# Kernel optimization log

Measured on AMD Instinct MI355X. Metric: run time of the kernel, lower is better.

The kernel has to match this reference:

```python
import jax, jax.numpy as jnp
from jax import lax
import numpy as np

G = 33            # LUT grid size per axis (hard-coded in module)
G3 = G * G * G    # 35937 entries per channel LUT


def _gelu(x):
    return jax.nn.gelu(x, approximate=False)  # torch nn.GELU default = exact erf


def _conv(x, w, b):
    # 3x3 stride-1 padding-1 conv == SAME padding, NCHW/OIHW like torch
    y = lax.conv_general_dilated(x, w, (1, 1), 'SAME',
                                 dimension_numbers=('NCHW', 'OIHW', 'NCHW'))
    return y + b[None, :, None, None]


def _bn(x, g, b, eps=1e-5):
    # eval-mode BatchNorm2d with running_mean=0, running_var=1
    s = g * (1.0 + eps) ** -0.5
    return x * s[None, :, None, None] + b[None, :, None, None]


def _resblock(x, wA, bA, gA, btA, wB, bB, gB, btB):
    h = _gelu(_bn(_conv(x, wA, bA), gA, btA))
    h = _bn(_conv(h, wB, bB), gB, btB)
    return _gelu(h + x)


def _apply_luts(luts_flat, recon):
    # Trilinear 3D-LUT sampling == F.grid_sample(mode='bilinear', padding_mode='border',
    # align_corners=True) on a 5D LUT. grid = recon[...,[2,1,0]]*2-1 means image ch0 (R)
    # indexes LUT dim 2, ch1 (G) dim 3, ch2 (B) dim 4; align_corners maps v->v*(G-1).
    # luts_flat: [B, L*3, G^3] (all num_luts fused into the channel dim, gathered once)
    # recon:     [B, 3, H, W] in [0,1]
    B, C3, _ = luts_flat.shape
    _, _, H, W = recon.shape
    c = jnp.clip(recon * (G - 1.0), 0.0, G - 1.0)      # border clamp
    f0 = jnp.clip(jnp.floor(c), 0.0, G - 2.0)
    t = c - f0                                          # fractional weights [B,3,H,W]
    i0 = f0.astype(jnp.int32)
    r0, g0, b0 = i0[:, 0], i0[:, 1], i0[:, 2]           # [B,H,W] each
    tr, tg, tb = t[:, 0], t[:, 1], t[:, 2]
    out = jnp.zeros((B, C3, H * W), dtype=luts_flat.dtype)
    for dr in (0, 1):
        for dg in (0, 1):
            for db in (0, 1):
                idx = ((r0 + dr) * G + (g0 + dg)) * G + (b0 + db)   # [B,H,W]
                w = ((tr if dr else 1.0 - tr) * (tg if dg else 1.0 - tg)
                     * (tb if db else 1.0 - tb))
                vals = jnp.take_along_axis(luts_flat, idx.reshape(B, 1, H * W), axis=2)
                out = out + vals * w.reshape(B, 1, H * W)
    return out.reshape(B, C3 // 3, 3, H, W)            # [B, L, 3, H, W]


def setup_inputs() -> dict:
    key = jax.random.key(0)
    ks = iter(jax.random.split(key, 32))
    def nrm(shape, s=0.02):
        return jax.random.normal(next(ks), shape, jnp.float32) * s
    B, T, V, E, HID, L, H, W = 4, 1024, 1024, 256, 256, 8, 384, 384
    inp = dict(
        tokens=jax.random.randint(next(ks), (B, T), 0, V),
        img=jax.random.uniform(next(ks), (B, 3, H, W), jnp.float32),
        recon_image=jax.random.uniform(next(ks), (B, 3, H, W), jnp.float32),
        emb_table=nrm((V, E)),
        agg_w1=nrm((E, HID)), agg_b1=jnp.zeros((HID,), jnp.float32),
        agg_w2=nrm((HID, HID)), agg_b2=jnp.zeros((HID,), jnp.float32),
        lut_w1=nrm((HID, HID)), lut_b1=jnp.zeros((HID,), jnp.float32),
        lut_w2=nrm((HID, L * 3 * G3), 0.005),
        lut_b2=jnp.zeros((L * 3 * G3,), jnp.float32),
        wg_w1=nrm((HID, HID // 4)), wg_b1=jnp.zeros((HID // 4,), jnp.float32),
        wg_w2=nrm((HID // 4, L)), wg_b2=jnp.zeros((L,), jnp.float32),
        rp_cin_w=nrm((32, 3, 3, 3)), rp_cin_b=jnp.zeros((32,), jnp.float32),
        rp_rbA_w=nrm((32, 32, 3, 3)), rp_rbA_b=jnp.zeros((32,), jnp.float32),
        rp_rbA_g=jnp.ones((32,), jnp.float32), rp_rbA_bt=jnp.zeros((32,), jnp.float32),
        rp_rbB_w=nrm((32, 32, 3, 3)), rp_rbB_b=jnp.zeros((32,), jnp.float32),
        rp_rbB_g=jnp.ones((32,), jnp.float32), rp_rbB_bt=jnp.zeros((32,), jnp.float32),
        rp_cout_w=nrm((3, 32, 3, 3)), rp_cout_b=jnp.zeros((3,), jnp.float32),
        fu_cin_w=nrm((32, 6, 3, 3)), fu_cin_b=jnp.zeros((32,), jnp.float32),
        fu_rbA_w=nrm((32, 32, 3, 3)), fu_rbA_b=jnp.zeros((32,), jnp.float32),
        fu_rbA_g=jnp.ones((32,), jnp.float32), fu_rbA_bt=jnp.zeros((32,), jnp.float32),
        fu_rbB_w=nrm((32, 32, 3, 3)), fu_rbB_b=jnp.zeros((32,), jnp.float32),
        fu_rbB_g=jnp.ones((32,), jnp.float32), fu_rbB_bt=jnp.zeros((32,), jnp.float32),
        fu_cout_w=nrm((3, 32, 3, 3)), fu_cout_b=jnp.zeros((3,), jnp.float32),
    )
    return inp


def reference(tokens, img, recon_image, emb_table,
              agg_w1, agg_b1, agg_w2, agg_b2,
              lut_w1, lut_b1, lut_w2, lut_b2,
              wg_w1, wg_b1, wg_w2, wg_b2,
              rp_cin_w, rp_cin_b, rp_rbA_w, rp_rbA_b, rp_rbA_g, rp_rbA_bt,
              rp_rbB_w, rp_rbB_b, rp_rbB_g, rp_rbB_bt, rp_cout_w, rp_cout_b,
              fu_cin_w, fu_cin_b, fu_rbA_w, fu_rbA_b, fu_rbA_g, fu_rbA_bt,
              fu_rbB_w, fu_rbB_b, fu_rbB_g, fu_rbB_bt, fu_cout_w, fu_cout_b):
    B = img.shape[0]
    L = wg_w2.shape[1]
    # token features
    emb = emb_table[tokens]                       # [B, T, E]
    tf = jnp.mean(emb, axis=1)                    # [B, E]
    tf = _gelu(tf @ agg_w1 + agg_b1) @ agg_w2 + agg_b2   # [B, HID]
    # dynamic LUTs and fusion weights
    lut_params = _gelu(tf @ lut_w1 + lut_b1) @ lut_w2 + lut_b2   # [B, L*3*G3]
    luts_flat = lut_params.reshape(B, L * 3, G3)
    lw = jax.nn.softmax(_gelu(tf @ wg_w1 + wg_b1) @ wg_w2 + wg_b2, axis=1)  # [B, L]
    # apply all LUTs in one fused gather pass, then weighted sum over LUTs
    lut_out = _apply_luts(luts_flat, recon_image)                # [B, L, 3, H, W]
    fused = jnp.einsum('blchw,bl->bchw', lut_out, lw)            # [B, 3, H, W]
    # residual processing branch on original img
    proc = _gelu(_conv(img, rp_cin_w, rp_cin_b))
    proc = _resblock(proc, rp_rbA_w, rp_rbA_b, rp_rbA_g, rp_rbA_bt,
                     rp_rbB_w, rp_rbB_b, rp_rbB_g, rp_rbB_bt)
    proc = _conv(proc, rp_cout_w, rp_cout_b)
    # fusion
    comb = jnp.concatenate([fused, proc], axis=1)                # [B, 6, H, W]
    out = _gelu(_conv(comb, fu_cin_w, fu_cin_b))
    out = _resblock(out, fu_rbA_w, fu_rbA_b, fu_rbA_g, fu_rbA_bt,
                    fu_rbB_w, fu_rbB_b, fu_rbB_g, fu_rbB_bt)
    out = _conv(out, fu_cout_w, fu_cout_b)
    return out + img
```

## Files before the change

### kernel.cpp

```cpp
#include <hip/hip_runtime.h>
#include <hip/hip_bf16.h>
#include <math.h>

#define BB    4
#define TT    1024
#define EE    256
#define HIDD  256
#define LLUT  8
#define HGT   384
#define WID   384
#define HWPX  147456
#define GSZ   33
#define G3    35937
#define NCOL  862488

typedef __attribute__((ext_vector_type(8))) short bf16x8;
typedef __attribute__((ext_vector_type(4))) float f32x4;

__device__ __forceinline__ float gelu_f(float x) {
    float s = 1.5957691216057308f * x * (1.0f + 0.044715f * x * x);
    float e = __expf(s);
    return x - x / (e + 1.0f);
}

__device__ __forceinline__ ushort f2bf(float x) {
    uint u = __float_as_uint(x);
    return (ushort)((u + 0x7FFFu + ((u >> 16) & 1u)) >> 16);
}
__device__ __forceinline__ uint pack2bf(float a, float b) {
    return (uint)f2bf(a) | ((uint)f2bf(b) << 16);
}
__device__ __forceinline__ float bf2f_lo(uint u) { return __uint_as_float(u << 16); }
__device__ __forceinline__ float bf2f_hi(uint u) { return __uint_as_float(u & 0xFFFF0000u); }

__global__ __launch_bounds__(256) void emb_partial_kernel(
    const int* __restrict__ tokens, const float* __restrict__ emb,
    float* __restrict__ partial)
{
    const int s = blockIdx.x, b = blockIdx.y, tid = threadIdx.x;
    const int* tok = tokens + b * TT + s * 16;
    float acc = 0.f;
#pragma unroll
    for (int t = 0; t < 16; ++t) acc += emb[tok[t] * EE + tid];
    partial[(b * 64 + s) * EE + tid] = acc;
}

__global__ __launch_bounds__(1024) void mlp_head_kernel(
    const float* __restrict__ partial,
    const float* __restrict__ aw1, const float* __restrict__ ab1,
    const float* __restrict__ aw2, const float* __restrict__ ab2,
    const float* __restrict__ lw1, const float* __restrict__ lb1,
    const float* __restrict__ gw1, const float* __restrict__ gb1,
    const float* __restrict__ gw2, const float* __restrict__ gb2,
    float* __restrict__ h3_out, float* __restrict__ lw_out)
{
    const int b = blockIdx.x;
    const int tid = threadIdx.x;
    const int o = tid & 255;
    const int q = tid >> 8;
    __shared__ float tf[256], h1[256], tf2s[256], h4[64], lg[8];
    __shared__ float red[4][256];

    {
        float acc = 0.f;
#pragma unroll
        for (int s = 0; s < 16; ++s)
            acc += partial[(b * 64 + q * 16 + s) * EE + o];
        red[q][o] = acc;
    }
    __syncthreads();
    if (tid < 256)
        tf[tid] = (red[0][tid] + red[1][tid] + red[2][tid] + red[3][tid]) * (1.0f / TT);
    __syncthreads();

    {
        float s = 0.f;
#pragma unroll 8
        for (int j = 0; j < 64; ++j) {
            const int k = (q << 6) + j;
            s += tf[k] * aw1[k * HIDD + o];
        }
        red[q][o] = s;
    }
    __syncthreads();
    if (tid < 256)
        h1[tid] = gelu_f(red[0][tid] + red[1][tid] + red[2][tid] + red[3][tid] + ab1[tid]);
    __syncthreads();

    {
        float s = 0.f;
#pragma unroll 8
        for (int j = 0; j < 64; ++j) {
            const int k = (q << 6) + j;
            s += h1[k] * aw2[k * HIDD + o];
        }
        red[q][o] = s;
    }
    __syncthreads();
    if (tid < 256)
        tf2s[tid] = red[0][tid] + red[1][tid] + red[2][tid] + red[3][tid] + ab2[tid];
    __syncthreads();

    {
        float s = 0.f;
#pragma unroll 8
        for (int j = 0; j < 64; ++j) {
            const int k = (q << 6) + j;
            s += tf2s[k] * lw1[k * HIDD + o];
        }
        red[q][o] = s;
    }
    __syncthreads();
    if (tid < 256)
        h3_out[b * HIDD + tid] =
            gelu_f(red[0][tid] + red[1][tid] + red[2][tid] + red[3][tid] + lb1[tid]);
    __syncthreads();

    {
        const int o64 = tid & 63, q16 = tid >> 6;
        float s = 0.f;
#pragma unroll
        for (int j = 0; j < 16; ++j) {
            const int k = q16 * 16 + j;
            s += tf2s[k] * gw1[k * 64 + o64];
        }
        ((float*)red)[q16 * 64 + o64] = s;
    }
    __syncthreads();
    if (tid < 64) {
        float s = gb1[tid];
#pragma unroll
        for (int r = 0; r < 16; ++r) s += ((float*)red)[r * 64 + tid];
        h4[tid] = gelu_f(s);
    }
    __syncthreads();

    if (tid < 8) {
        float s = gb2[tid];
#pragma unroll 8
        for (int k = 0; k < 64; ++k) s += h4[k] * gw2[k * LLUT + tid];
        lg[tid] = s;
    }
    __syncthreads();
    if (tid == 0) {
        float m = lg[0];
        for (int i = 1; i < LLUT; ++i) m = fmaxf(m, lg[i]);
        float ssum = 0.f, ex[LLUT];
        for (int i = 0; i < LLUT; ++i) { ex[i] = expf(lg[i] - m); ssum += ex[i]; }
        for (int i = 0; i < LLUT; ++i) lw_out[b * LLUT + i] = ex[i] / ssum;
    }
}

__global__ __launch_bounds__(256) void lut_gemm_kernel(
    const float* __restrict__ h3, const float* __restrict__ w2,
    const float* __restrict__ b2, float* __restrict__ lp)
{
    __shared__ float h[BB * HIDD];
    const int tid = threadIdx.x;
    for (int i = tid; i < BB * HIDD; i += 256) h[i] = h3[i];
    __syncthreads();

    const long col = ((long)blockIdx.x * 256 + tid) * 4;
    if (col >= NCOL) return;

    const float4 bias = *(const float4*)(b2 + col);
    float4 a0 = bias, a1 = bias, a2 = bias, a3 = bias;
    const float* wp = w2 + col;
#pragma unroll 4
    for (int k = 0; k < HIDD; ++k) {
        float4 w = *(const float4*)(wp + (long)k * NCOL);
        float h0 = h[k], h1v = h[HIDD + k], h2 = h[2 * HIDD + k], h3v = h[3 * HIDD + k];
        a0.x += h0 * w.x;  a0.y += h0 * w.y;  a0.z += h0 * w.z;  a0.w += h0 * w.w;
        a1.x += h1v * w.x; a1.y += h1v * w.y; a1.z += h1v * w.z; a1.w += h1v * w.w;
        a2.x += h2 * w.x;  a2.y += h2 * w.y;  a2.z += h2 * w.z;  a2.w += h2 * w.w;
        a3.x += h3v * w.x; a3.y += h3v * w.y; a3.z += h3v * w.z; a3.w += h3v * w.w;
    }
    *(float4*)(lp + 0L * NCOL + col) = a0;
    *(float4*)(lp + 1L * NCOL + col) = a1;
    *(float4*)(lp + 2L * NCOL + col) = a2;
    *(float4*)(lp + 3L * NCOL + col) = a3;
}

__global__ __launch_bounds__(256) void combine_kernel(
    const float* __restrict__ lp, const float* __restrict__ lwv,
    float* __restrict__ clut)
{
    const int v = blockIdx.x * 256 + threadIdx.x;
    const int b = blockIdx.y;
    if (v >= G3) return;
    float w[LLUT];
#pragma unroll
    for (int l = 0; l < LLUT; ++l) w[l] = lwv[b * LLUT + l];
#pragma unroll
    for (int c = 0; c < 3; ++c) {
        float s = 0.f;
#pragma unroll
        for (int l = 0; l < LLUT; ++l)
            s += w[l] * lp[(long)b * NCOL + (long)(l * 3 + c) * G3 + v];
        clut[(long)(b * 3 + c) * G3 + v] = s;
    }
}

__global__ __launch_bounds__(256) void applylut_out3_kernel(
    const float* __restrict__ clut, const float* __restrict__ recon,
    const ushort* __restrict__ act2, const float* __restrict__ wgt,
    const float* __restrict__ bias, float* __restrict__ comb)
{
    const int p = blockIdx.x * 256 + threadIdx.x;
    const int b = blockIdx.y;

    const float* rc = recon + (long)b * 3 * HWPX;
    float cr = fminf(fmaxf(rc[p] * 32.f, 0.f), 32.f);
    float cg = fminf(fmaxf(rc[HWPX + p] * 32.f, 0.f), 32.f);
    float cb = fminf(fmaxf(rc[2 * HWPX + p] * 32.f, 0.f), 32.f);
    float fr = fminf(floorf(cr), 31.f);
    float fg = fminf(floorf(cg), 31.f);
    float fb = fminf(floorf(cb), 31.f);
    float tr = cr - fr, tg = cg - fg, tb_ = cb - fb;
    int idx = (((int)fr * GSZ + (int)fg) * GSZ + (int)fb);
    float c[3];
#pragma unroll
    for (int ch = 0; ch < 3; ++ch) {
        const float* lut = clut + (long)(b * 3 + ch) * G3;
        float v000 = lut[idx],                  v001 = lut[idx + 1];
        float v010 = lut[idx + GSZ],            v011 = lut[idx + GSZ + 1];
        float v100 = lut[idx + GSZ * GSZ],      v101 = lut[idx + GSZ * GSZ + 1];
        float v110 = lut[idx + GSZ * GSZ + GSZ], v111 = lut[idx + GSZ * GSZ + GSZ + 1];
        float c00 = v000 + (v001 - v000) * tb_;
        float c01 = v010 + (v011 - v010) * tb_;
        float c10 = v100 + (v101 - v100) * tb_;
        float c11 = v110 + (v111 - v110) * tb_;
        float c0 = c00 + (c01 - c00) * tg;
        float c1 = c10 + (c11 - c10) * tg;
        c[ch] = c0 + (c1 - c0) * tr;
    }
    float4 r4; r4.x = c[0]; r4.y = c[1]; r4.z = c[2]; r4.w = 0.f;
    *(float4*)(comb + ((long)b * HWPX + p) * 8) = r4;

    const int hh = p / WID, ww = p - hh * WID;
    float acc[3] = {bias[0], bias[1], bias[2]};
#pragma unroll
    for (int tap = 0; tap < 9; ++tap) {
        const int dh = tap / 3, dw = tap - dh * 3;
        const int gh = hh + dh - 1, gw = ww + dw - 1;
        if (gh < 0 || gh >= HGT || gw < 0 || gw >= WID) continue;
        const uint4* xp = (const uint4*)(act2 + ((long)b * HWPX + gh * WID + gw) * 32);
        float xx[32];
#pragma unroll
        for (int q = 0; q < 4; ++q) {
            uint4 v = xp[q];
            xx[q * 8 + 0] = bf2f_lo(v.x); xx[q * 8 + 1] = bf2f_hi(v.x);
            xx[q * 8 + 2] = bf2f_lo(v.y); xx[q * 8 + 3] = bf2f_hi(v.y);
            xx[q * 8 + 4] = bf2f_lo(v.z); xx[q * 8 + 5] = bf2f_hi(v.z);
            xx[q * 8 + 6] = bf2f_lo(v.w); xx[q * 8 + 7] = bf2f_hi(v.w);
        }
#pragma unroll
        for (int o = 0; o < 3; ++o)
#pragma unroll
            for (int ci = 0; ci < 32; ++ci)
                acc[o] += xx[ci] * wgt[o * 288 + ci * 9 + tap];
    }
    float4 s4; s4.x = acc[0]; s4.y = acc[1]; s4.z = acc[2]; s4.w = 0.f;
    *(float4*)(comb + ((long)b * HWPX + p) * 8 + 4) = s4;
}

__global__ __launch_bounds__(256) void conv_in3_kernel(
    const float* __restrict__ img, const float* __restrict__ wgt,
    const float* __restrict__ bias, ushort* __restrict__ out)
{
    const int tid = threadIdx.x;
    const int p0 = (blockIdx.x * 256 + tid) * 2;
    const int b = blockIdx.y;
    const int hh = p0 / WID, ww = p0 - hh * WID;

    float acc[32][2];
#pragma unroll
    for (int o = 0; o < 32; ++o) { float bv = bias[o]; acc[o][0] = bv; acc[o][1] = bv; }

    const bool wlo = (ww > 0), whi = (ww + 2 < WID);
#pragma unroll
    for (int ci = 0; ci < 3; ++ci) {
        const float* ip = img + (long)(b * 3 + ci) * HWPX;
        float x[3][4];
#pragma unroll
        for (int dh = 0; dh < 3; ++dh) {
            const int hs = hh + dh - 1;
            const bool hok = (hs >= 0) && (hs < HGT);
            const float* rp_ = ip + hs * WID + ww;
            x[dh][0] = (hok && wlo) ? rp_[-1] : 0.f;
            x[dh][1] = hok ? rp_[0] : 0.f;
            x[dh][2] = hok ? rp_[1] : 0.f;
            x[dh][3] = (hok && whi) ? rp_[2] : 0.f;
        }
#pragma unroll
        for (int o = 0; o < 32; ++o) {
            const float* wv = wgt + o * 27 + ci * 9;
#pragma unroll
            for (int dh = 0; dh < 3; ++dh)
#pragma unroll
                for (int dw = 0; dw < 3; ++dw) {
                    const float w = wv[dh * 3 + dw];
                    acc[o][0] += x[dh][dw]     * w;
                    acc[o][1] += x[dh][dw + 1] * w;
                }
        }
    }

    ushort* op = out + ((long)b * HWPX + p0) * 32;
#pragma unroll
    for (int px = 0; px < 2; ++px) {
        uint u[16];
#pragma unroll
        for (int o2 = 0; o2 < 16; ++o2)
            u[o2] = pack2bf(gelu_f(acc[2 * o2][px]), gelu_f(acc[2 * o2 + 1][px]));
        uint4* dst = (uint4*)(op + px * 32);
#pragma unroll
        for (int q = 0; q < 4; ++q)
            dst[q] = make_uint4(u[4 * q], u[4 * q + 1], u[4 * q + 2], u[4 * q + 3]);
    }
}

#define TH2 8
#define TW2 64
#define HALO_H2 10
#define HALO_W2 66
#define CSTR 40

template <bool HAS_RES>
__global__ __launch_bounds__(512, 4) void conv32_mfma(
    const ushort* __restrict__ in, const ushort* __restrict__ res,
    const float* __restrict__ wgt, const float* __restrict__ bias,
    const float* __restrict__ bn_g, const float* __restrict__ bn_bt,
    ushort* __restrict__ out)
{
    __shared__ ushort halo[HALO_H2 * HALO_W2 * CSTR];
    __shared__ ushort wlA[9 * 2 * 64 * 8];
    __shared__ float s_scale[32], s_shift[32];

    const int tid = threadIdx.x;
    const int b  = blockIdx.z;
    const int h0 = blockIdx.y * TH2;
    const int w0 = blockIdx.x * TW2;

    for (int i = tid; i < 9 * 2 * 64 * 8; i += 512) {
        const int j    = i & 7;
        const int lane_= (i >> 3) & 63;
        const int half = (i >> 9) & 1;
        const int tap  = i >> 10;
        const int co = half * 16 + (lane_ & 15);
        const int ci = (lane_ >> 4) * 8 + j;
        wlA[i] = f2bf(wgt[co * 288 + ci * 9 + tap]);
    }
    if (tid < 32) {
        float sg = bn_g[tid] * 0.9999950000375f;
        s_scale[tid] = sg;
        s_shift[tid] = bias[tid] * sg + bn_bt[tid];
    }

    const ushort* inb = in + (long)b * HWPX * 32;
    for (int i = tid; i < HALO_H2 * HALO_W2 * 4; i += 512) {
        const int row = i / (HALO_W2 * 4);
        const int rem = i - row * (HALO_W2 * 4);
        const int px = rem >> 2, q = rem & 3;
        const int gh = h0 + row - 1, gw = w0 + px - 1;
        uint4 v = make_uint4(0u, 0u, 0u, 0u);
        if (gh >= 0 && gh < HGT && gw >= 0 && gw < WID)
            v = *(const uint4*)(inb + ((long)gh * WID + gw) * 32 + q * 8);
        *(uint4*)(&halo[(row * HALO_W2 + px) * CSTR + q * 8]) = v;
    }
    __syncthreads();

    const int lane = tid & 63, wid = tid >> 6;
    const int l15 = lane & 15, kg = lane >> 4;
    const int r = wid;

    f32x4 acc[4][2];
#pragma unroll
    for (int f = 0; f < 4; ++f)
#pragma unroll
        for (int cf = 0; cf < 2; ++cf)
            acc[f][cf] = (f32x4){0.f, 0.f, 0.f, 0.f};

#pragma unroll
    for (int tap = 0; tap < 9; ++tap) {
        const int dh = tap / 3, dw = tap - dh * 3;
        const bf16x8 a0 = *(const bf16x8*)(&wlA[((tap * 2 + 0) * 64 + lane) * 8]);
        const bf16x8 a1 = *(const bf16x8*)(&wlA[((tap * 2 + 1) * 64 + lane) * 8]);
#pragma unroll
        for (int f = 0; f < 4; ++f) {
            const int c0 = f * 16;
            const bf16x8 bfv = *(const bf16x8*)(
                &halo[((r + dh) * HALO_W2 + (c0 + dw + l15)) * CSTR + kg * 8]);
            acc[f][0] = __builtin_amdgcn_mfma_f32_16x16x32_bf16(a0, bfv, acc[f][0], 0, 0, 0);
            acc[f][1] = __builtin_amdgcn_mfma_f32_16x16x32_bf16(a1, bfv, acc[f][1], 0, 0, 0);
        }
    }

#pragma unroll
    for (int f = 0; f < 4; ++f) {
        const int c0 = f * 16;
        const long gpx = (long)b * HWPX + (long)(h0 + r) * WID + (w0 + c0 + l15);
#pragma unroll
        for (int cf = 0; cf < 2; ++cf) {
            const int co0 = cf * 16 + kg * 4;
            const float4 sc = *(const float4*)(&s_scale[co0]);
            const float4 sh = *(const float4*)(&s_shift[co0]);
            float v0 = acc[f][cf][0] * sc.x + sh.x;
            float v1 = acc[f][cf][1] * sc.y + sh.y;
            float v2 = acc[f][cf][2] * sc.z + sh.z;
            float v3 = acc[f][cf][3] * sc.w + sh.w;
            if (HAS_RES) {
                const uint2 rv = *(const uint2*)(res + gpx * 32 + co0);
                v0 += bf2f_lo(rv.x); v1 += bf2f_hi(rv.x);
                v2 += bf2f_lo(rv.y); v3 += bf2f_hi(rv.y);
            }
            uint2 o;
            o.x = pack2bf(gelu_f(v0), gelu_f(v1));
            o.y = pack2bf(gelu_f(v2), gelu_f(v3));
            *(uint2*)(out + gpx * 32 + co0) = o;
        }
    }
}

__global__ __launch_bounds__(256) void conv_in6_kernel(
    const float* __restrict__ comb, const float* __restrict__ wgt,
    const float* __restrict__ bias, ushort* __restrict__ out)
{
    const int p = blockIdx.x * 256 + threadIdx.x;
    const int b = blockIdx.y;
    const int hh = p / WID, ww = p - hh * WID;

    float acc[32];
#pragma unroll
    for (int o = 0; o < 32; ++o) acc[o] = bias[o];

#pragma unroll
    for (int tap = 0; tap < 9; ++tap) {
        const int dh = tap / 3, dw = tap - dh * 3;
        const int gh = hh + dh - 1, gw = ww + dw - 1;
        if (gh < 0 || gh >= HGT || gw < 0 || gw >= WID) continue;
        const float4* cp = (const float4*)(comb + ((long)b * HWPX + gh * WID + gw) * 8);
        const float4 qa = cp[0], qb = cp[1];
        const float xs[6] = {qa.x, qa.y, qa.z, qb.x, qb.y, qb.z};
#pragma unroll
        for (int o = 0; o < 32; ++o) {
            const float* wv = wgt + o * 54 + tap;
            acc[o] += xs[0] * wv[0]  + xs[1] * wv[9]  + xs[2] * wv[18]
                    + xs[3] * wv[27] + xs[4] * wv[36] + xs[5] * wv[45];
        }
    }

    ushort* op = out + ((long)b * HWPX + p) * 32;
    uint u[16];
#pragma unroll
    for (int o2 = 0; o2 < 16; ++o2)
        u[o2] = pack2bf(gelu_f(acc[2 * o2]), gelu_f(acc[2 * o2 + 1]));
    uint4* dst = (uint4*)op;
#pragma unroll
    for (int q = 0; q < 4; ++q)
        dst[q] = make_uint4(u[4 * q], u[4 * q + 1], u[4 * q + 2], u[4 * q + 3]);
}

__global__ __launch_bounds__(256) void conv_final_kernel(
    const ushort* __restrict__ in, const float* __restrict__ wgt,
    const float* __restrict__ bias, const float* __restrict__ img,
    float* __restrict__ outp)
{
    const int p = blockIdx.x * 256 + threadIdx.x;
    const int b = blockIdx.y;
    const int hh = p / WID, ww = p - hh * WID;
    float acc[3] = {bias[0], bias[1], bias[2]};

#pragma unroll
    for (int tap = 0; tap < 9; ++tap) {
        const int dh = tap / 3, dw = tap - dh * 3;
        const int gh = hh + dh - 1, gw = ww + dw - 1;
        if (gh < 0 || gh >= HGT || gw < 0 || gw >= WID) continue;
        const uint4* xp = (const uint4*)(in + ((long)b * HWPX + gh * WID + gw) * 32);
        float xx[32];
#pragma unroll
        for (int q = 0; q < 4; ++q) {
            uint4 v = xp[q];
            xx[q * 8 + 0] = bf2f_lo(v.x); xx[q * 8 + 1] = bf2f_hi(v.x);
            xx[q * 8 + 2] = bf2f_lo(v.y); xx[q * 8 + 3] = bf2f_hi(v.y);
            xx[q * 8 + 4] = bf2f_lo(v.z); xx[q * 8 + 5] = bf2f_hi(v.z);
            xx[q * 8 + 6] = bf2f_lo(v.w); xx[q * 8 + 7] = bf2f_hi(v.w);
        }
#pragma unroll
        for (int o = 0; o < 3; ++o)
#pragma unroll
            for (int ci = 0; ci < 32; ++ci)
                acc[o] += xx[ci] * wgt[o * 288 + ci * 9 + tap];
    }
#pragma unroll
    for (int o = 0; o < 3; ++o)
        outp[(long)(b * 3 + o) * HWPX + p] = acc[o] + img[(long)(b * 3 + o) * HWPX + p];
}

extern "C" void kernel_launch(void* const* d_in, const int* in_sizes, int n_in,
                              void* d_out, int out_size, void* d_ws, size_t ws_size,
                              hipStream_t stream)
{
    const int*   tokens  = (const int*)d_in[0];
    const float* img     = (const float*)d_in[1];
    const float* recon   = (const float*)d_in[2];
    const float* emb     = (const float*)d_in[3];
    const float* agg_w1  = (const float*)d_in[4];
    const float* agg_b1  = (const float*)d_in[5];
    const float* agg_w2  = (const float*)d_in[6];
    const float* agg_b2  = (const float*)d_in[7];
    const float* lut_w1  = (const float*)d_in[8];
    const float* lut_b1  = (const float*)d_in[9];
    const float* lut_w2  = (const float*)d_in[10];
    const float* lut_b2  = (const float*)d_in[11];
    const float* wg_w1   = (const float*)d_in[12];
    const float* wg_b1   = (const float*)d_in[13];
    const float* wg_w2   = (const float*)d_in[14];
    const float* wg_b2   = (const float*)d_in[15];
    const float* rp_cin_w = (const float*)d_in[16];
    const float* rp_cin_b = (const float*)d_in[17];
    const float* rp_rbA_w = (const float*)d_in[18];
    const float* rp_rbA_b = (const float*)d_in[19];
    const float* rp_rbA_g = (const float*)d_in[20];
    const float* rp_rbA_bt= (const float*)d_in[21];
    const float* rp_rbB_w = (const float*)d_in[22];
    const float* rp_rbB_b = (const float*)d_in[23];
    const float* rp_rbB_g = (const float*)d_in[24];
    const float* rp_rbB_bt= (const float*)d_in[25];
    const float* rp_cout_w= (const float*)d_in[26];
    const float* rp_cout_b= (const float*)d_in[27];
    const float* fu_cin_w = (const float*)d_in[28];
    const float* fu_cin_b = (const float*)d_in[29];
    const float* fu_rbA_w = (const float*)d_in[30];
    const float* fu_rbA_b = (const float*)d_in[31];
    const float* fu_rbA_g = (const float*)d_in[32];
    const float* fu_rbA_bt= (const float*)d_in[33];
    const float* fu_rbB_w = (const float*)d_in[34];
    const float* fu_rbB_b = (const float*)d_in[35];
    const float* fu_rbB_g = (const float*)d_in[36];
    const float* fu_rbB_bt= (const float*)d_in[37];
    const float* fu_cout_w= (const float*)d_in[38];
    const float* fu_cout_b= (const float*)d_in[39];

    float* ws = (float*)d_ws;
    float*  h3      = ws;
    float*  lwv     = ws + 1024;
    float*  partial = ws + 2048;
    float*  lp      = ws + 69632;
    float*  clut    = ws + 3519584;
    float*  comb    = ws + 3952640;
    ushort* act0    = (ushort*)(ws + 8675328);
    ushort* act1    = (ushort*)(ws + 18112512);
    ushort* act2    = (ushort*)(ws + 27549696);
    float*  outp    = (float*)d_out;

    emb_partial_kernel<<<dim3(64, BB), dim3(256), 0, stream>>>(tokens, emb, partial);
    mlp_head_kernel<<<dim3(BB), dim3(1024), 0, stream>>>(
        partial, agg_w1, agg_b1, agg_w2, agg_b2,
        lut_w1, lut_b1, wg_w1, wg_b1, wg_w2, wg_b2, h3, lwv);

    lut_gemm_kernel<<<dim3((NCOL / 4 + 255) / 256), dim3(256), 0, stream>>>(
        h3, lut_w2, lut_b2, lp);
    combine_kernel<<<dim3((G3 + 255) / 256, BB), dim3(256), 0, stream>>>(lp, lwv, clut);

    const dim3 g1(HWPX / 256, BB), g2(HWPX / 512, BB), blk(256);
    const dim3 gm(WID / TW2, HGT / TH2, BB), bm(512);

    conv_in3_kernel<<<g2, blk, 0, stream>>>(img, rp_cin_w, rp_cin_b, act0);
    conv32_mfma<false><<<gm, bm, 0, stream>>>(
        act0, nullptr, rp_rbA_w, rp_rbA_b, rp_rbA_g, rp_rbA_bt, act1);
    conv32_mfma<true><<<gm, bm, 0, stream>>>(
        act1, act0, rp_rbB_w, rp_rbB_b, rp_rbB_g, rp_rbB_bt, act2);

    applylut_out3_kernel<<<g1, blk, 0, stream>>>(
        clut, recon, act2, rp_cout_w, rp_cout_b, comb);

    conv_in6_kernel<<<g1, blk, 0, stream>>>(comb, fu_cin_w, fu_cin_b, act0);
    conv32_mfma<false><<<gm, bm, 0, stream>>>(
        act0, nullptr, fu_rbA_w, fu_rbA_b, fu_rbA_g, fu_rbA_bt, act1);
    conv32_mfma<true><<<gm, bm, 0, stream>>>(
        act1, act0, fu_rbB_w, fu_rbB_b, fu_rbB_g, fu_rbB_bt, act2);
    conv_final_kernel<<<g1, blk, 0, stream>>>(act2, fu_cout_w, fu_cout_b, img, outp);
}
```

Measured before the change: 563.6 us.

## Use zero-padded activation buffers and two-pixel-per-thread direct convs

Stores all intermediate activations (act0/1/2, comb) in a 386x386 layout with a one-pixel zero border, written once by a new border-zeroing kernel. The convolution kernels then drop their per-tap bounds checks and halo predication. The scalar 3-out and 6-in convolutions now compute two adjacent pixels per thread, so the overlapping 4-column window is loaded and unpacked once for both outputs. This trades an extra small launch and a slightly larger workspace for less redundant global loading and branching.

```diff
diff --git a/kernel.cpp b/kernel.cpp
--- a/kernel.cpp
+++ b/kernel.cpp
@@ -14,6 +14,10 @@
 #define G3    35937
 #define NCOL  862488
 
+#define PW    386
+#define PHW   148996
+#define RINGN 1540
+
 typedef __attribute__((ext_vector_type(8))) short bf16x8;
 typedef __attribute__((ext_vector_type(4))) float f32x4;
 
@@ -32,6 +36,41 @@
 }
 __device__ __forceinline__ float bf2f_lo(uint u) { return __uint_as_float(u << 16); }
 __device__ __forceinline__ float bf2f_hi(uint u) { return __uint_as_float(u & 0xFFFF0000u); }
+
+__device__ __forceinline__ void unpack32(const uint4* xp, float* xx) {
+#pragma unroll
+    for (int q = 0; q < 4; ++q) {
+        uint4 v = xp[q];
+        xx[q * 8 + 0] = bf2f_lo(v.x); xx[q * 8 + 1] = bf2f_hi(v.x);
+        xx[q * 8 + 2] = bf2f_lo(v.y); xx[q * 8 + 3] = bf2f_hi(v.y);
+        xx[q * 8 + 4] = bf2f_lo(v.z); xx[q * 8 + 5] = bf2f_hi(v.z);
+        xx[q * 8 + 6] = bf2f_lo(v.w); xx[q * 8 + 7] = bf2f_hi(v.w);
+    }
+}
+
+__global__ __launch_bounds__(256) void zero_border_kernel(
+    ushort* __restrict__ a0, ushort* __restrict__ a1, ushort* __restrict__ a2,
+    float* __restrict__ comb)
+{
+    const int r = blockIdx.x * 256 + threadIdx.x;
+    if (r >= RINGN) return;
+    const int b = blockIdx.y;
+    const int buf = blockIdx.z;
+    int row, col;
+    if (r < PW)            { row = 0;      col = r; }
+    else if (r < 2 * PW)   { row = PW - 1; col = r - PW; }
+    else { int rem = r - 2 * PW; row = 1 + (rem >> 1); col = (rem & 1) ? (PW - 1) : 0; }
+    const long px = (long)b * PHW + (long)row * PW + col;
+    if (buf < 3) {
+        ushort* p = (buf == 0 ? a0 : buf == 1 ? a1 : a2) + px * 32;
+        const uint4 z = make_uint4(0u, 0u, 0u, 0u);
+        ((uint4*)p)[0] = z; ((uint4*)p)[1] = z; ((uint4*)p)[2] = z; ((uint4*)p)[3] = z;
+    } else {
+        float4 z4; z4.x = z4.y = z4.z = z4.w = 0.f;
+        float* p = comb + px * 8;
+        ((float4*)p)[0] = z4; ((float4*)p)[1] = z4;
+    }
+}
 
 __global__ __launch_bounds__(256) void emb_partial_kernel(
     const int* __restrict__ tokens, const float* __restrict__ emb,
@@ -206,62 +245,80 @@
     const ushort* __restrict__ act2, const float* __restrict__ wgt,
     const float* __restrict__ bias, float* __restrict__ comb)
 {
-    const int p = blockIdx.x * 256 + threadIdx.x;
+    const int p0 = (blockIdx.x * 256 + threadIdx.x) * 2;
     const int b = blockIdx.y;
-
+    const int hh = p0 / WID, ww = p0 - hh * WID;
+
+    float lut_out[2][3];
     const float* rc = recon + (long)b * 3 * HWPX;
-    float cr = fminf(fmaxf(rc[p] * 32.f, 0.f), 32.f);
-    float cg = fminf(fmaxf(rc[HWPX + p] * 32.f, 0.f), 32.f);
-    float cb = fminf(fmaxf(rc[2 * HWPX + p] * 32.f, 0.f), 32.f);
-    float fr = fminf(floorf(cr), 31.f);
-    float fg = fminf(floorf(cg), 31.f);
-    float fb = fminf(floorf(cb), 31.f);
-    float tr = cr - fr, tg = cg - fg, tb_ = cb - fb;
-    int idx = (((int)fr * GSZ + (int)fg) * GSZ + (int)fb);
-    float c[3];
-#pragma unroll
-    for (int ch = 0; ch < 3; ++ch) {
-        const float* lut = clut + (long)(b * 3 + ch) * G3;
-        float v000 = lut[idx],                  v001 = lut[idx + 1];
-        float v010 = lut[idx + GSZ],            v011 = lut[idx + GSZ + 1];
-        float v100 = lut[idx + GSZ * GSZ],      v101 = lut[idx + GSZ * GSZ + 1];
-        float v110 = lut[idx + GSZ * GSZ + GSZ], v111 = lut[idx + GSZ * GSZ + GSZ + 1];
-        float c00 = v000 + (v001 - v000) * tb_;
-        float c01 = v010 + (v011 - v010) * tb_;
-        float c10 = v100 + (v101 - v100) * tb_;
-        float c11 = v110 + (v111 - v110) * tb_;
-        float c0 = c00 + (c01 - c00) * tg;
-        float c1 = c10 + (c11 - c10) * tg;
-        c[ch] = c0 + (c1 - c0) * tr;
-    }
-    float4 r4; r4.x = c[0]; r4.y = c[1]; r4.z = c[2]; r4.w = 0.f;
-    *(float4*)(comb + ((long)b * HWPX + p) * 8) = r4;
-
-    const int hh = p / WID, ww = p - hh * WID;
-    float acc[3] = {bias[0], bias[1], bias[2]};
-#pragma unroll
-    for (int tap = 0; tap < 9; ++tap) {
-        const int dh = tap / 3, dw = tap - dh * 3;
-        const int gh = hh + dh - 1, gw = ww + dw - 1;
-        if (gh < 0 || gh >= HGT || gw < 0 || gw >= WID) continue;
-        const uint4* xp = (const uint4*)(act2 + ((long)b * HWPX + gh * WID + gw) * 32);
-        float xx[32];
-#pragma unroll
-        for (int q = 0; q < 4; ++q) {
-            uint4 v = xp[q];
-            xx[q * 8 + 0] = bf2f_lo(v.x); xx[q * 8 + 1] = bf2f_hi(v.x);
-            xx[q * 8 + 2] = bf2f_lo(v.y); xx[q * 8 + 3] = bf2f_hi(v.y);
-            xx[q * 8 + 4] = bf2f_lo(v.z); xx[q * 8 + 5] = bf2f_hi(v.z);
-            xx[q * 8 + 6] = bf2f_lo(v.w); xx[q * 8 + 7] = bf2f_hi(v.w);
-        }
-#pragma unroll
-        for (int o = 0; o < 3; ++o)
-#pragma unroll
-            for (int ci = 0; ci < 32; ++ci)
-                acc[o] += xx[ci] * wgt[o * 288 + ci * 9 + tap];
-    }
-    float4 s4; s4.x = acc[0]; s4.y = acc[1]; s4.z = acc[2]; s4.w = 0.f;
-    *(float4*)(comb + ((long)b * HWPX + p) * 8 + 4) = s4;
+    const float2 rr = *(const float2*)(rc + p0);
+    const float2 rg = *(const float2*)(rc + HWPX + p0);
+    const float2 rb = *(const float2*)(rc + 2 * HWPX + p0);
+#pragma unroll
+    for (int px = 0; px < 2; ++px) {
+        float cr = fminf(fmaxf((px ? rr.y : rr.x) * 32.f, 0.f), 32.f);
+        float cg = fminf(fmaxf((px ? rg.y : rg.x) * 32.f, 0.f), 32.f);
+        float cb = fminf(fmaxf((px ? rb.y : rb.x) * 32.f, 0.f), 32.f);
+        float fr = fminf(floorf(cr), 31.f);
+        float fg = fminf(floorf(cg), 31.f);
+        float fb = fminf(floorf(cb), 31.f);
+        float tr = cr - fr, tg = cg - fg, tb_ = cb - fb;
+        int idx = (((int)fr * GSZ + (int)fg) * GSZ + (int)fb);
+#pragma unroll
+        for (int ch = 0; ch < 3; ++ch) {
+            const float* lut = clut + (long)(b * 3 + ch) * G3;
+            float v000 = lut[idx],                   v001 = lut[idx + 1];
+            float v010 = lut[idx + GSZ],             v011 = lut[idx + GSZ + 1];
+            float v100 = lut[idx + GSZ * GSZ],       v101 = lut[idx + GSZ * GSZ + 1];
+            float v110 = lut[idx + GSZ * GSZ + GSZ], v111 = lut[idx + GSZ * GSZ + GSZ + 1];
+            float c00 = v000 + (v001 - v000) * tb_;
+            float c01 = v010 + (v011 - v010) * tb_;
+            float c10 = v100 + (v101 - v100) * tb_;
+            float c11 = v110 + (v111 - v110) * tb_;
+            float c0 = c00 + (c01 - c00) * tg;
+            float c1 = c10 + (c11 - c10) * tg;
+            lut_out[px][ch] = c0 + (c1 - c0) * tr;
+        }
+    }
+
+    float a0[3] = {bias[0], bias[1], bias[2]};
+    float a1[3] = {bias[0], bias[1], bias[2]};
+#pragma unroll
+    for (int dh = 0; dh < 3; ++dh) {
+        const ushort* rp = act2 + ((long)b * PHW + (long)(hh + dh) * PW + ww) * 32;
+#pragma unroll
+        for (int c = 0; c < 4; ++c) {
+            float xx[32];
+            unpack32((const uint4*)(rp + c * 32), xx);
+            if (c < 3) {
+                const int tap = dh * 3 + c;
+#pragma unroll
+                for (int o = 0; o < 3; ++o)
+#pragma unroll
+                    for (int ci = 0; ci < 32; ++ci)
+                        a0[o] += xx[ci] * wgt[o * 288 + ci * 9 + tap];
+            }
+            if (c > 0) {
+                const int tap = dh * 3 + c - 1;
+#pragma unroll
+                for (int o = 0; o < 3; ++o)
+#pragma unroll
+                    for (int ci = 0; ci < 32; ++ci)
+                        a1[o] += xx[ci] * wgt[o * 288 + ci * 9 + tap];
+            }
+        }
+    }
+
+    float* cb = comb + ((long)b * PHW + (long)(hh + 1) * PW + (ww + 1)) * 8;
+    float4 r4;
+    r4.x = lut_out[0][0]; r4.y = lut_out[0][1]; r4.z = lut_out[0][2]; r4.w = 0.f;
+    *(float4*)(cb + 0) = r4;
+    r4.x = a0[0]; r4.y = a0[1]; r4.z = a0[2]; r4.w = 0.f;
+    *(float4*)(cb + 4) = r4;
+    r4.x = lut_out[1][0]; r4.y = lut_out[1][1]; r4.z = lut_out[1][2]; r4.w = 0.f;
+    *(float4*)(cb + 8) = r4;
+    r4.x = a1[0]; r4.y = a1[1]; r4.z = a1[2]; r4.w = 0.f;
+    *(float4*)(cb + 12) = r4;
 }
 
 __global__ __launch_bounds__(256) void conv_in3_kernel(
@@ -306,7 +363,7 @@
         }
     }
 
-    ushort* op = out + ((long)b * HWPX + p0) * 32;
+    ushort* op = out + ((long)b * PHW + (long)(hh + 1) * PW + (ww + 1)) * 32;
 #pragma unroll
     for (int px = 0; px < 2; ++px) {
         uint u[16];
@@ -357,15 +414,12 @@
         s_shift[tid] = bias[tid] * sg + bn_bt[tid];
     }
 
-    const ushort* inb = in + (long)b * HWPX * 32;
+    const ushort* inb = in + (long)b * PHW * 32;
     for (int i = tid; i < HALO_H2 * HALO_W2 * 4; i += 512) {
         const int row = i / (HALO_W2 * 4);
         const int rem = i - row * (HALO_W2 * 4);
         const int px = rem >> 2, q = rem & 3;
-        const int gh = h0 + row - 1, gw = w0 + px - 1;
-        uint4 v = make_uint4(0u, 0u, 0u, 0u);
-        if (gh >= 0 && gh < HGT && gw >= 0 && gw < WID)
-            v = *(const uint4*)(inb + ((long)gh * WID + gw) * 32 + q * 8);
+        uint4 v = *(const uint4*)(inb + ((long)(h0 + row) * PW + (w0 + px)) * 32 + q * 8);
         *(uint4*)(&halo[(row * HALO_W2 + px) * CSTR + q * 8]) = v;
     }
     __syncthreads();
@@ -399,7 +453,7 @@
 #pragma unroll
     for (int f = 0; f < 4; ++f) {
         const int c0 = f * 16;
-        const long gpx = (long)b * HWPX + (long)(h0 + r) * WID + (w0 + c0 + l15);
+        const long gpx = (long)b * PHW + (long)(h0 + r + 1) * PW + (w0 + c0 + l15 + 1);
 #pragma unroll
         for (int cf = 0; cf < 2; ++cf) {
             const int co0 = cf * 16 + kg * 4;
@@ -426,39 +480,64 @@
     const float* __restrict__ comb, const float* __restrict__ wgt,
     const float* __restrict__ bias, ushort* __restrict__ out)
 {
-    const int p = blockIdx.x * 256 + threadIdx.x;
+    const int p0 = (blockIdx.x * 256 + threadIdx.x) * 2;
     const int b = blockIdx.y;
-    const int hh = p / WID, ww = p - hh * WID;
-
-    float acc[32];
-#pragma unroll
-    for (int o = 0; o < 32; ++o) acc[o] = bias[o];
-
-#pragma unroll
-    for (int tap = 0; tap < 9; ++tap) {
-        const int dh = tap / 3, dw = tap - dh * 3;
-        const int gh = hh + dh - 1, gw = ww + dw - 1;
-        if (gh < 0 || gh >= HGT || gw < 0 || gw >= WID) continue;
-        const float4* cp = (const float4*)(comb + ((long)b * HWPX + gh * WID + gw) * 8);
-        const float4 qa = cp[0], qb = cp[1];
-        const float xs[6] = {qa.x, qa.y, qa.z, qb.x, qb.y, qb.z};
-#pragma unroll
-        for (int o = 0; o < 32; ++o) {
-            const float* wv = wgt + o * 54 + tap;
-            acc[o] += xs[0] * wv[0]  + xs[1] * wv[9]  + xs[2] * wv[18]
-                    + xs[3] * wv[27] + xs[4] * wv[36] + xs[5] * wv[45];
-        }
-    }
-
-    ushort* op = out + ((long)b * HWPX + p) * 32;
-    uint u[16];
-#pragma unroll
-    for (int o2 = 0; o2 < 16; ++o2)
-        u[o2] = pack2bf(gelu_f(acc[2 * o2]), gelu_f(acc[2 * o2 + 1]));
-    uint4* dst = (uint4*)op;
-#pragma unroll
-    for (int q = 0; q < 4; ++q)
-        dst[q] = make_uint4(u[4 * q], u[4 * q + 1], u[4 * q + 2], u[4 * q + 3]);
+    const int hh = p0 / WID, ww = p0 - hh * WID;
+
+    float a0[32], a1[32];
+#pragma unroll
+    for (int o = 0; o < 32; ++o) { float bv = bias[o]; a0[o] = bv; a1[o] = bv; }
+
+#pragma unroll
+    for (int dh = 0; dh < 3; ++dh) {
+        const float* cp = comb + ((long)b * PHW + (long)(hh + dh) * PW + ww) * 8;
+#pragma unroll
+        for (int c = 0; c < 4; ++c) {
+            const float4 qa = *(const float4*)(cp + c * 8);
+            const float4 qb = *(const float4*)(cp + c * 8 + 4);
+            const float xs[6] = {qa.x, qa.y, qa.z, qb.x, qb.y, qb.z};
+            if (c < 3) {
+                const int tap = dh * 3 + c;
+#pragma unroll
+                for (int o = 0; o < 32; ++o) {
+                    const float* wv = wgt + o * 54 + tap;
+                    a0[o] += xs[0] * wv[0]  + xs[1] * wv[9]  + xs[2] * wv[18]
+                           + xs[3] * wv[27] + xs[4] * wv[36] + xs[5] * wv[45];
+                }
+            }
+            if (c > 0) {
+                const int tap = dh * 3 + c - 1;
+#pragma unroll
+                for (int o = 0; o < 32; ++o) {
+                    const float* wv = wgt + o * 54 + tap;
+                    a1[o] += xs[0] * wv[0]  + xs[1] * wv[9]  + xs[2] * wv[18]
+                           + xs[3] * wv[27] + xs[4] * wv[36] + xs[5] * wv[45];
+                }
+            }
+        }
+    }
+
+    ushort* op = out + ((long)b * PHW + (long)(hh + 1) * PW + (ww + 1)) * 32;
+    {
+        uint u[16];
+#pragma unroll
+        for (int o2 = 0; o2 < 16; ++o2)
+            u[o2] = pack2bf(gelu_f(a0[2 * o2]), gelu_f(a0[2 * o2 + 1]));
+        uint4* dst = (uint4*)op;
+#pragma unroll
+        for (int q = 0; q < 4; ++q)
+            dst[q] = make_uint4(u[4 * q], u[4 * q + 1], u[4 * q + 2], u[4 * q + 3]);
+    }
+    {
+        uint u[16];
+#pragma unroll
+        for (int o2 = 0; o2 < 16; ++o2)
+            u[o2] = pack2bf(gelu_f(a1[2 * o2]), gelu_f(a1[2 * o2 + 1]));
+        uint4* dst = (uint4*)(op + 32);
+#pragma unroll
+        for (int q = 0; q < 4; ++q)
+            dst[q] = make_uint4(u[4 * q], u[4 * q + 1], u[4 * q + 2], u[4 * q + 3]);
+    }
 }
 
 __global__ __launch_bounds__(256) void conv_final_kernel(
@@ -466,35 +545,44 @@
     const float* __restrict__ bias, const float* __restrict__ img,
     float* __restrict__ outp)
 {
-    const int p = blockIdx.x * 256 + threadIdx.x;
+    const int p0 = (blockIdx.x * 256 + threadIdx.x) * 2;
     const int b = blockIdx.y;
-    const int hh = p / WID, ww = p - hh * WID;
-    float acc[3] = {bias[0], bias[1], bias[2]};
-
-#pragma unroll
-    for (int tap = 0; tap < 9; ++tap) {
-        const int dh = tap / 3, dw = tap - dh * 3;
-        const int gh = hh + dh - 1, gw = ww + dw - 1;
-        if (gh < 0 || gh >= HGT || gw < 0 || gw >= WID) continue;
-        const uint4* xp = (const uint4*)(in + ((long)b * HWPX + gh * WID + gw) * 32);
-        float xx[32];
-#pragma unroll
-        for (int q = 0; q < 4; ++q) {
-            uint4 v = xp[q];
-            xx[q * 8 + 0] = bf2f_lo(v.x); xx[q * 8 + 1] = bf2f_hi(v.x);
-            xx[q * 8 + 2] = bf2f_lo(v.y); xx[q * 8 + 3] = bf2f_hi(v.y);
-            xx[q * 8 + 4] = bf2f_lo(v.z); xx[q * 8 + 5] = bf2f_hi(v.z);
-            xx[q * 8 + 6] = bf2f_lo(v.w); xx[q * 8 + 7] = bf2f_hi(v.w);
-        }
-#pragma unroll
-        for (int o = 0; o < 3; ++o)
-#pragma unroll
-            for (int ci = 0; ci < 32; ++ci)
-                acc[o] += xx[ci] * wgt[o * 288 + ci * 9 + tap];
-    }
-#pragma unroll
-    for (int o = 0; o < 3; ++o)
-        outp[(long)(b * 3 + o) * HWPX + p] = acc[o] + img[(long)(b * 3 + o) * HWPX + p];
+    const int hh = p0 / WID, ww = p0 - hh * WID;
+
+    float a0[3] = {bias[0], bias[1], bias[2]};
+    float a1[3] = {bias[0], bias[1], bias[2]};
+
+#pragma unroll
+    for (int dh = 0; dh < 3; ++dh) {
+        const ushort* rp = in + ((long)b * PHW + (long)(hh + dh) * PW + ww) * 32;
+#pragma unroll
+        for (int c = 0; c < 4; ++c) {
+            float xx[32];
+            unpack32((const uint4*)(rp + c * 32), xx);
+            if (c < 3) {
+                const int tap = dh * 3 + c;
+#pragma unroll
+                for (int o = 0; o < 3; ++o)
+#pragma unroll
+                    for (int ci = 0; ci < 32; ++ci)
+                        a0[o] += xx[ci] * wgt[o * 288 + ci * 9 + tap];
+            }
+            if (c > 0) {
+                const int tap = dh * 3 + c - 1;
+#pragma unroll
+                for (int o = 0; o < 3; ++o)
+#pragma unroll
+                    for (int ci = 0; ci < 32; ++ci)
+                        a1[o] += xx[ci] * wgt[o * 288 + ci * 9 + tap];
+            }
+        }
+    }
+#pragma unroll
+    for (int o = 0; o < 3; ++o) {
+        const float2 iv = *(const float2*)(img + (long)(b * 3 + o) * HWPX + p0);
+        float2 ov; ov.x = a0[o] + iv.x; ov.y = a1[o] + iv.y;
+        *(float2*)(outp + (long)(b * 3 + o) * HWPX + p0) = ov;
+    }
 }
 
 extern "C" void kernel_launch(void* const* d_in, const int* in_sizes, int n_in,
@@ -549,10 +637,12 @@
     float*  lp      = ws + 69632;
     float*  clut    = ws + 3519584;
     float*  comb    = ws + 3952640;
-    ushort* act0    = (ushort*)(ws + 8675328);
-    ushort* act1    = (ushort*)(ws + 18112512);
-    ushort* act2    = (ushort*)(ws + 27549696);
+    ushort* act0    = (ushort*)(ws + 8720512);
+    ushort* act1    = (ushort*)(ws + 18256256);
+    ushort* act2    = (ushort*)(ws + 27792000);
     float*  outp    = (float*)d_out;
+
+    zero_border_kernel<<<dim3(7, BB, 4), dim3(256), 0, stream>>>(act0, act1, act2, comb);
 
     emb_partial_kernel<<<dim3(64, BB), dim3(256), 0, stream>>>(tokens, emb, partial);
     mlp_head_kernel<<<dim3(BB), dim3(1024), 0, stream>>>(
@@ -563,7 +653,7 @@
         h3, lut_w2, lut_b2, lp);
     combine_kernel<<<dim3((G3 + 255) / 256, BB), dim3(256), 0, stream>>>(lp, lwv, clut);
 
-    const dim3 g1(HWPX / 256, BB), g2(HWPX / 512, BB), blk(256);
+    const dim3 g2(HWPX / 512, BB), blk(256);
     const dim3 gm(WID / TW2, HGT / TH2, BB), bm(512);
 
     conv_in3_kernel<<<g2, blk, 0, stream>>>(img, rp_cin_w, rp_cin_b, act0);
@@ -572,13 +662,13 @@
     conv32_mfma<true><<<gm, bm, 0, stream>>>(
         act1, act0, rp_rbB_w, rp_rbB_b, rp_rbB_g, rp_rbB_bt, act2);
 
-    applylut_out3_kernel<<<g1, blk, 0, stream>>>(
+    applylut_out3_kernel<<<g2, blk, 0, stream>>>(
         clut, recon, act2, rp_cout_w, rp_cout_b, comb);
 
-    conv_in6_kernel<<<g1, blk, 0, stream>>>(comb, fu_cin_w, fu_cin_b, act0);
+    conv_in6_kernel<<<g2, blk, 0, stream>>>(comb, fu_cin_w, fu_cin_b, act0);
     conv32_mfma<false><<<gm, bm, 0, stream>>>(
         act0, nullptr, fu_rbA_w, fu_rbA_b, fu_rbA_g, fu_rbA_bt, act1);
     conv32_mfma<true><<<gm, bm, 0, stream>>>(
         act1, act0, fu_rbB_w, fu_rbB_b, fu_rbB_g, fu_rbB_bt, act2);
-    conv_final_kernel<<<g1, blk, 0, stream>>>(act2, fu_cout_w, fu_cout_b, img, outp);
-}
+    conv_final_kernel<<<g2, blk, 0, stream>>>(act2, fu_cout_w, fu_cout_b, img, outp);
+}
```

Result: slower. 1.356 ms (+140.5%).

## Fuse LUT GEMM with LUT-weight combine and remap conv blocks across XCDs

Applied to the files above, without the earlier changes.

The LUT projection GEMM and the softmax-weighted LUT combine are merged into one kernel. Each thread computes all 8 LUT outputs for one (channel, vertex) and reduces them on the fly, so the large intermediate lp buffer is never written to or read back from global memory. The conv32 kernels switch to a 1D grid with a block-index swizzle so neighbouring tiles land on the same XCD, aiming for better L2 reuse of halos. The fused kernel loses float4 loads, keeps 32 accumulators per thread, and launches fewer threads, which may reduce memory-level parallelism.

```diff
diff --git a/kernel.cpp b/kernel.cpp
--- a/kernel.cpp
+++ b/kernel.cpp
@@ -151,52 +151,52 @@
     }
 }
 
-__global__ __launch_bounds__(256) void lut_gemm_kernel(
-    const float* __restrict__ h3, const float* __restrict__ w2,
-    const float* __restrict__ b2, float* __restrict__ lp)
+__global__ __launch_bounds__(256) void lut_fused_kernel(
+    const float* __restrict__ h3, const float* __restrict__ lwv,
+    const float* __restrict__ w2, const float* __restrict__ b2,
+    float* __restrict__ clut)
 {
     __shared__ float h[BB * HIDD];
+    __shared__ float lws[BB * LLUT];
     const int tid = threadIdx.x;
     for (int i = tid; i < BB * HIDD; i += 256) h[i] = h3[i];
-    __syncthreads();
-
-    const long col = ((long)blockIdx.x * 256 + tid) * 4;
-    if (col >= NCOL) return;
-
-    const float4 bias = *(const float4*)(b2 + col);
-    float4 a0 = bias, a1 = bias, a2 = bias, a3 = bias;
-    const float* wp = w2 + col;
+    if (tid < BB * LLUT) lws[tid] = lwv[tid];
+    __syncthreads();
+
+    const int idx = blockIdx.x * 256 + tid;
+    if (idx >= 3 * G3) return;
+    const int c = idx / G3, v = idx - c * G3;
+
+    float acc[BB][LLUT];
+#pragma unroll
+    for (int b = 0; b < BB; ++b)
+#pragma unroll
+        for (int l = 0; l < LLUT; ++l) acc[b][l] = 0.f;
+
+    const float* wbase = w2 + (long)c * G3 + v;
 #pragma unroll 4
     for (int k = 0; k < HIDD; ++k) {
-        float4 w = *(const float4*)(wp + (long)k * NCOL);
-        float h0 = h[k], h1v = h[HIDD + k], h2 = h[2 * HIDD + k], h3v = h[3 * HIDD + k];
-        a0.x += h0 * w.x;  a0.y += h0 * w.y;  a0.z += h0 * w.z;  a0.w += h0 * w.w;
-        a1.x += h1v * w.x; a1.y += h1v * w.y; a1.z += h1v * w.z; a1.w += h1v * w.w;
-        a2.x += h2 * w.x;  a2.y += h2 * w.y;  a2.z += h2 * w.z;  a2.w += h2 * w.w;
-        a3.x += h3v * w.x; a3.y += h3v * w.y; a3.z += h3v * w.z; a3.w += h3v * w.w;
-    }
-    *(float4*)(lp + 0L * NCOL + col) = a0;
-    *(float4*)(lp + 1L * NCOL + col) = a1;
-    *(float4*)(lp + 2L * NCOL + col) = a2;
-    *(float4*)(lp + 3L * NCOL + col) = a3;
-}
-
-__global__ __launch_bounds__(256) void combine_kernel(
-    const float* __restrict__ lp, const float* __restrict__ lwv,
-    float* __restrict__ clut)
-{
-    const int v = blockIdx.x * 256 + threadIdx.x;
-    const int b = blockIdx.y;
-    if (v >= G3) return;
-    float w[LLUT];
-#pragma unroll
-    for (int l = 0; l < LLUT; ++l) w[l] = lwv[b * LLUT + l];
-#pragma unroll
-    for (int c = 0; c < 3; ++c) {
+        const float* row = wbase + (long)k * NCOL;
+        float wl[LLUT];
+#pragma unroll
+        for (int l = 0; l < LLUT; ++l) wl[l] = row[l * 3 * G3];
+#pragma unroll
+        for (int b = 0; b < BB; ++b) {
+            const float hb = h[b * HIDD + k];
+#pragma unroll
+            for (int l = 0; l < LLUT; ++l) acc[b][l] += wl[l] * hb;
+        }
+    }
+
+    float bb[LLUT];
+#pragma unroll
+    for (int l = 0; l < LLUT; ++l) bb[l] = b2[(long)(l * 3 + c) * G3 + v];
+
+#pragma unroll
+    for (int b = 0; b < BB; ++b) {
         float s = 0.f;
 #pragma unroll
-        for (int l = 0; l < LLUT; ++l)
-            s += w[l] * lp[(long)b * NCOL + (long)(l * 3 + c) * G3 + v];
+        for (int l = 0; l < LLUT; ++l) s += lws[b * LLUT + l] * (acc[b][l] + bb[l]);
         clut[(long)(b * 3 + c) * G3 + v] = s;
     }
 }
@@ -322,6 +322,10 @@
 
 #define TH2 8
 #define TW2 64
+#define NTX (WID / TW2)
+#define NTY (HGT / TH2)
+#define NBLK (NTX * NTY * BB)
+#define CHUNK (NBLK / 8)
 #define HALO_H2 10
 #define HALO_W2 66
 #define CSTR 40
@@ -338,9 +342,14 @@
     __shared__ float s_scale[32], s_shift[32];
 
     const int tid = threadIdx.x;
-    const int b  = blockIdx.z;
-    const int h0 = blockIdx.y * TH2;
-    const int w0 = blockIdx.x * TW2;
+    const int bid = blockIdx.x;
+    const int t   = (bid & 7) * CHUNK + (bid >> 3);
+    const int tx  = t % NTX;
+    const int rem = t / NTX;
+    const int ty  = rem % NTY;
+    const int b   = rem / NTY;
+    const int h0 = ty * TH2;
+    const int w0 = tx * TW2;
 
     for (int i = tid; i < 9 * 2 * 64 * 8; i += 512) {
         const int j    = i & 7;
@@ -360,8 +369,8 @@
     const ushort* inb = in + (long)b * HWPX * 32;
     for (int i = tid; i < HALO_H2 * HALO_W2 * 4; i += 512) {
         const int row = i / (HALO_W2 * 4);
-        const int rem = i - row * (HALO_W2 * 4);
-        const int px = rem >> 2, q = rem & 3;
+        const int rem2 = i - row * (HALO_W2 * 4);
+        const int px = rem2 >> 2, q = rem2 & 3;
         const int gh = h0 + row - 1, gw = w0 + px - 1;
         uint4 v = make_uint4(0u, 0u, 0u, 0u);
         if (gh >= 0 && gh < HGT && gw >= 0 && gw < WID)
@@ -546,12 +555,11 @@
     float*  h3      = ws;
     float*  lwv     = ws + 1024;
     float*  partial = ws + 2048;
-    float*  lp      = ws + 69632;
-    float*  clut    = ws + 3519584;
-    float*  comb    = ws + 3952640;
-    ushort* act0    = (ushort*)(ws + 8675328);
-    ushort* act1    = (ushort*)(ws + 18112512);
-    ushort* act2    = (ushort*)(ws + 27549696);
+    float*  clut    = ws + 69632;
+    float*  comb    = ws + 524288;
+    ushort* act0    = (ushort*)(ws + 5242880);
+    ushort* act1    = (ushort*)(ws + 14680064);
+    ushort* act2    = (ushort*)(ws + 24117248);
     float*  outp    = (float*)d_out;
 
     emb_partial_kernel<<<dim3(64, BB), dim3(256), 0, stream>>>(tokens, emb, partial);
@@ -559,12 +567,11 @@
         partial, agg_w1, agg_b1, agg_w2, agg_b2,
         lut_w1, lut_b1, wg_w1, wg_b1, wg_w2, wg_b2, h3, lwv);
 
-    lut_gemm_kernel<<<dim3((NCOL / 4 + 255) / 256), dim3(256), 0, stream>>>(
-        h3, lut_w2, lut_b2, lp);
-    combine_kernel<<<dim3((G3 + 255) / 256, BB), dim3(256), 0, stream>>>(lp, lwv, clut);
+    lut_fused_kernel<<<dim3((3 * G3 + 255) / 256), dim3(256), 0, stream>>>(
+        h3, lwv, lut_w2, lut_b2, clut);
 
     const dim3 g1(HWPX / 256, BB), g2(HWPX / 512, BB), blk(256);
-    const dim3 gm(WID / TW2, HGT / TH2, BB), bm(512);
+    const dim3 gm(NBLK), bm(512);
 
     conv_in3_kernel<<<g2, blk, 0, stream>>>(img, rp_cin_w, rp_cin_b, act0);
     conv32_mfma<false><<<gm, bm, 0, stream>>>(
```

Measured after the change: 564.3 us. About the same (+0.1%).
